# Optimization experiments

Hardware: AMD Instinct MI355X
Metric: run time of the kernel (lower is better)

## Reference

```python
import jax, jax.numpy as jnp
import numpy as np

DIM = 768
NUM_HEADS = 12
HEAD_DIM = DIM // NUM_HEADS
SCALE = HEAD_DIM ** -0.5
EPS = 1e-6


def setup_inputs() -> dict:
    key = jax.random.key(0)
    k_x, k_p, k_qkv, k_proj = jax.random.split(key, 4)
    B, N = 16, 577
    x = jax.random.normal(k_x, (B, N, DIM), dtype=jnp.float32)
    # binary keep/drop policy per token (as produced by an upstream gumbel gate)
    policy = jax.random.randint(k_p, (B, N, 1), 0, 2).astype(jnp.float32)
    Wqkv = jax.random.normal(k_qkv, (DIM, 3 * DIM), dtype=jnp.float32) * 0.02
    bqkv = jnp.zeros((3 * DIM,), dtype=jnp.float32)
    Wproj = jax.random.normal(k_proj, (DIM, DIM), dtype=jnp.float32) * 0.02
    bproj = jnp.zeros((DIM,), dtype=jnp.float32)
    return {"x": x, "policy": policy, "Wqkv": Wqkv, "bqkv": bqkv,
            "Wproj": Wproj, "bproj": bproj}


def reference(x, policy, Wqkv, bqkv, Wproj, bproj):
    B, N, C = x.shape
    # qkv projection -> [3, B, H, N, Dh]
    qkv = (x @ Wqkv + bqkv).reshape(B, N, 3, NUM_HEADS, HEAD_DIM)
    qkv = jnp.transpose(qkv, (2, 0, 3, 1, 4))
    q, k, v = qkv[0], qkv[1], qkv[2]
    # scaled attention logits [B, H, N, N]
    attn = jnp.einsum("bhnd,bhmd->bhnm", q, k) * SCALE
    # policy-masked softmax (training-mode formula: eye keeps self-attention alive)
    ap = policy.reshape(B, 1, 1, N)
    eye = jnp.eye(N, dtype=ap.dtype).reshape(1, 1, N, N)
    ap = ap + (1.0 - ap) * eye
    max_att = jnp.max(attn, axis=-1, keepdims=True)
    e = jnp.exp(attn - max_att) * ap
    attn = (e + EPS / N) / (jnp.sum(e, axis=-1, keepdims=True) + EPS)
    # attend and project
    out = jnp.einsum("bhnm,bhmd->bhnd", attn, v)
    out = jnp.transpose(out, (0, 2, 1, 3)).reshape(B, N, C)
    return out @ Wproj + bproj
```

## Files before the change

kernel.cpp:

```cpp
#include <hip/hip_runtime.h>
#include <hip/hip_bf16.h>

#define QKVC   2304
#define NHEAD  12
#define NTOK   577
#define NBATCH 16
#define NROWS  (NBATCH * NTOK)
#define NPAD   640
#define SCALE  0.125f
#define EPSV   1e-6f

typedef __bf16  bf16x8 __attribute__((ext_vector_type(8)));
typedef float   f32x4  __attribute__((ext_vector_type(4)));

__device__ __forceinline__ unsigned short f2bf(float f) {
    union { float f; unsigned u; } v; v.f = f;
    unsigned r = v.u + 0x7FFFu + ((v.u >> 16) & 1u);
    return (unsigned short)(r >> 16);
}
__device__ __forceinline__ unsigned short f2bf_trunc(float f) {
    return (unsigned short)(__float_as_uint(f) >> 16);
}
__device__ __forceinline__ f32x4 mfma16(bf16x8 a, bf16x8 b, f32x4 c) {
    return __builtin_amdgcn_mfma_f32_16x16x32_bf16(a, b, c, 0, 0, 0);
}

#define GLDS16(g, l) __builtin_amdgcn_global_load_lds( \
    (const __attribute__((address_space(1))) unsigned int*)(g), \
    (__attribute__((address_space(3))) unsigned int*)(l), 16, 0, 0)

__device__ void transpose_tile(const float* __restrict__ src, unsigned short* __restrict__ dst,
                               int K, int N, int bx, int by, int t) {
    __shared__ unsigned short lt[64 * 72];
    int n0 = bx * 64, k0 = by * 64;
    int kk = t >> 4, nn = (t & 15) * 4;
    for (int i = 0; i < 4; i++) {
        int kr = kk + i * 16;
        float4 v = *(const float4*)&src[(size_t)(k0 + kr) * N + n0 + nn];
        lt[(nn + 0) * 72 + kr] = f2bf(v.x);
        lt[(nn + 1) * 72 + kr] = f2bf(v.y);
        lt[(nn + 2) * 72 + kr] = f2bf(v.z);
        lt[(nn + 3) * 72 + kr] = f2bf(v.w);
    }
    __syncthreads();
    int n = t >> 2, seg = (t & 3) * 16;
    uint4 a = *(uint4*)&lt[n * 72 + seg];
    uint4 b = *(uint4*)&lt[n * 72 + seg + 8];
    *(uint4*)&dst[(size_t)(n0 + n) * K + k0 + seg]     = a;
    *(uint4*)&dst[(size_t)(n0 + n) * K + k0 + seg + 8] = b;
}

#define NCONV (NROWS * 768 / 4 / 256)
__global__ void k_prep(const float* __restrict__ x, unsigned short* __restrict__ xb,
                       const float* __restrict__ Wqkv, unsigned short* __restrict__ wqkvt,
                       const float* __restrict__ Wproj, unsigned short* __restrict__ wprojt) {
    int id = blockIdx.x, t = threadIdx.x;
    if (id < NCONV) {
        int idx = id * 256 + t;
        float4 v = ((const float4*)x)[idx];
        ushort4 o;
        o.x = f2bf(v.x); o.y = f2bf(v.y); o.z = f2bf(v.z); o.w = f2bf(v.w);
        ((ushort4*)xb)[idx] = o;
    } else if (id < NCONV + 432) {
        int i2 = id - NCONV;
        transpose_tile(Wqkv, wqkvt, 768, QKVC, i2 % 36, i2 / 36, t);
    } else {
        int i2 = id - NCONV - 432;
        transpose_tile(Wproj, wprojt, 768, 768, i2 % 12, i2 / 12, t);
    }
}

template <bool F32OUT>
__global__ __launch_bounds__(256, 3)
void k_gemm(const unsigned short* __restrict__ A, const unsigned short* __restrict__ B,
            const float* __restrict__ bias, void* __restrict__ outp, int Ncols,
            unsigned short* __restrict__ vt) {
    __shared__ unsigned short SL[24576];
    unsigned short (*As)[4096] = (unsigned short (*)[4096])SL;
    unsigned short (*Bs)[4096] = (unsigned short (*)[4096])&SL[12288];
    int t = threadIdx.x;
    int lane = t & 63, wave = t >> 6, quad = lane >> 4, l15 = lane & 15;
    int wm = wave >> 1, wn = wave & 1;
    int nT = Ncols >> 7;
    int mLocal = blockIdx.x & 7;
    int rest = blockIdx.x >> 3;
    int n0 = (rest % nT) * 128;
    int m0 = ((rest / nT) * 8 + mLocal) * 128;

    const unsigned short* ga0 = A + (size_t)(m0 + wave * 32 + (lane >> 2)) * 768 + (lane & 3) * 8;
    const unsigned short* ga1 = ga0 + (size_t)16 * 768;
    const unsigned short* gb0 = B + (size_t)(n0 + wave * 32 + (lane >> 2)) * 768 + (lane & 3) * 8;
    const unsigned short* gb1 = gb0 + (size_t)16 * 768;
    unsigned lo = wave * 1024;

    f32x4 acc[4][4] = {};

    GLDS16(ga0,      &As[0][lo]); GLDS16(ga1,      &As[0][lo + 512]);
    GLDS16(gb0,      &Bs[0][lo]); GLDS16(gb1,      &Bs[0][lo + 512]);
    GLDS16(ga0 + 32, &As[1][lo]); GLDS16(ga1 + 32, &As[1][lo + 512]);
    GLDS16(gb0 + 32, &Bs[1][lo]); GLDS16(gb1 + 32, &Bs[1][lo + 512]);

    #pragma unroll 3
    for (int kt = 0; kt < 24; kt++) {
        int buf = kt % 3;
        if (kt == 23) { asm volatile("s_waitcnt vmcnt(0)" ::: "memory"); }
        else          { asm volatile("s_waitcnt vmcnt(4)" ::: "memory"); }
        asm volatile("s_barrier" ::: "memory");
        if (kt < 22) {
            int nb = buf + 2; if (nb >= 3) nb -= 3;
            int ko = (kt + 2) * 32;
            GLDS16(ga0 + ko, &As[nb][lo]); GLDS16(ga1 + ko, &As[nb][lo + 512]);
            GLDS16(gb0 + ko, &Bs[nb][lo]); GLDS16(gb1 + ko, &Bs[nb][lo + 512]);
        }
        bf16x8 af[4], bfr[4];
        for (int i = 0; i < 4; i++) {
            af[i]  = *(const bf16x8*)&As[buf][(wm * 64 + i * 16 + l15) * 32 + quad * 8];
            bfr[i] = *(const bf16x8*)&Bs[buf][(wn * 64 + i * 16 + l15) * 32 + quad * 8];
        }
        for (int mi = 0; mi < 4; mi++)
            for (int ni = 0; ni < 4; ni++)
                acc[mi][ni] = mfma16(af[mi], bfr[ni], acc[mi][ni]);
    }
    asm volatile("" ::: "memory");

    if constexpr (F32OUT) {
        for (int ni = 0; ni < 4; ni++) {
            int col = n0 + wn * 64 + ni * 16 + l15;
            float bv = bias[col];
            for (int mi = 0; mi < 4; mi++) {
                int rowm = m0 + wm * 64 + mi * 16 + quad * 4;
                for (int r = 0; r < 4; r++) {
                    int m = rowm + r;
                    if (m < NROWS)
                        ((float*)outp)[(size_t)m * Ncols + col] = acc[mi][ni][r] + bv;
                }
            }
        }
    } else {
        __syncthreads();
        for (int ni = 0; ni < 4; ni++) {
            int colL = wn * 64 + ni * 16 + l15;
            float bv = bias[n0 + colL];
            for (int mi = 0; mi < 4; mi++) {
                int rowL = wm * 64 + mi * 16 + quad * 4;
                for (int r = 0; r < 4; r++)
                    SL[(rowL + r) * 132 + colL] = f2bf(acc[mi][ni][r] + bv);
            }
        }
        __syncthreads();
        if (n0 < 1536) {
            for (int rr = 0; rr < 8; rr++) {
                int row = rr * 16 + (t >> 4);
                int m = m0 + row;
                if (m < NROWS) {
                    uint4 v = *(uint4*)&SL[row * 132 + (t & 15) * 8];
                    *(uint4*)&((unsigned short*)outp)[(size_t)m * Ncols + n0 + (t & 15) * 8] = v;
                }
            }
        } else {
            int h0 = (n0 - 1536) >> 6;
            for (int i = 0; i < 32; i++) {
                int c = wave * 32 + i;
                int h = h0 + (c >> 6), d = c & 63;
                for (int half = 0; half < 2; half++) {
                    int lr = half * 64 + lane;
                    int m = m0 + lr;
                    if (m < NROWS) {
                        unsigned bb = (unsigned)m / 577u;
                        int tok = m - (int)bb * 577;
                        vt[(((size_t)bb * NHEAD + h) * 64 + d) * NPAD + tok] =
                            SL[lr * 132 + c];
                    }
                }
            }
        }
    }
}

__global__ __launch_bounds__(256, 4)
void k_attn(const unsigned short* __restrict__ qkv, const unsigned short* __restrict__ vt,
            const float* __restrict__ policy, unsigned short* __restrict__ ao) {
    __shared__ unsigned short Ks[64 * 72];
    __shared__ unsigned short Vs[64 * 72];
    __shared__ unsigned short Ps[4][32 * 72];
    __shared__ float pol[NPAD];
    int t = threadIdx.x;
    int lane = t & 63, wave = t >> 6, quad = lane >> 4, l15 = lane & 15;
    int b = blockIdx.z, h = blockIdx.y, qt = blockIdx.x;
    const unsigned short* qbase = qkv + (size_t)(b * NTOK) * QKVC + h * 64;
    const unsigned short* kbase = qkv + (size_t)(b * NTOK) * QKVC + 768 + h * 64;
    const unsigned short* vbase = vt + (size_t)(b * NHEAD + h) * 64 * NPAD;

    for (int i = t; i < NPAD; i += 256)
        pol[i] = (i < NTOK) ? policy[b * NTOK + i] : 0.f;

    bf16x8 qf[2][2];
    for (int mi = 0; mi < 2; mi++) {
        const unsigned short* qp =
            qbase + (size_t)(qt * 128 + mi * 64 + wave * 16 + l15) * QKVC + quad * 8;
        qf[mi][0] = *(const bf16x8*)qp;
        qf[mi][1] = *(const bf16x8*)(qp + 32);
    }
    bf16x8 onesf;
    for (int j = 0; j < 8; j++) onesf[j] = (__bf16)1.0f;
    f32x4 o[2][4] = {};
    f32x4 ls[2] = {};
    int rowtok0[2];
    for (int mi = 0; mi < 2; mi++)
        rowtok0[mi] = qt * 128 + mi * 64 + wave * 16 + quad * 4;
    __syncthreads();

    for (int kt = 0; kt < 10; kt++) {
        int key0 = kt * 64;
        for (int i = t; i < 512; i += 256) {
            int row = i >> 3, seg = (i & 7) * 8;
            *(uint4*)&Ks[row * 72 + seg] = *(const uint4*)&kbase[(size_t)(key0 + row) * QKVC + seg];
            *(uint4*)&Vs[row * 72 + seg] = *(const uint4*)&vbase[(size_t)row * NPAD + key0 + seg];
        }
        __syncthreads();

        for (int ci = 0; ci < 4; ci++) {
            bf16x8 kf0 = *(const bf16x8*)&Ks[(ci * 16 + l15) * 72 + quad * 8];
            bf16x8 kf1 = *(const bf16x8*)&Ks[(ci * 16 + l15) * 72 + 32 + quad * 8];
            int col = key0 + ci * 16 + l15;
            float pc = pol[col];
            for (int mi = 0; mi < 2; mi++) {
                f32x4 a = {};
                a = mfma16(qf[mi][0], kf0, a);
                a = mfma16(qf[mi][1], kf1, a);
                for (int r = 0; r < 4; r++) {
                    float ap = (col == rowtok0[mi] + r) ? 1.f : pc;
                    float e = __expf(a[r] * SCALE) * ap;
                    Ps[wave][(mi * 16 + quad * 4 + r) * 72 + ci * 16 + l15] = f2bf_trunc(e);
                }
            }
        }
        __asm__ volatile("s_waitcnt lgkmcnt(0)" ::: "memory");
        bf16x8 pf[2][2];
        for (int mi = 0; mi < 2; mi++) {
            pf[mi][0] = *(const bf16x8*)&Ps[wave][(mi * 16 + l15) * 72 + quad * 8];
            pf[mi][1] = *(const bf16x8*)&Ps[wave][(mi * 16 + l15) * 72 + 32 + quad * 8];
            ls[mi] = mfma16(pf[mi][0], onesf, ls[mi]);
            ls[mi] = mfma16(pf[mi][1], onesf, ls[mi]);
        }
        for (int di = 0; di < 4; di++) {
            bf16x8 vf0 = *(const bf16x8*)&Vs[(di * 16 + l15) * 72 + quad * 8];
            bf16x8 vf1 = *(const bf16x8*)&Vs[(di * 16 + l15) * 72 + 32 + quad * 8];
            for (int mi = 0; mi < 2; mi++) {
                o[mi][di] = mfma16(pf[mi][0], vf0, o[mi][di]);
                o[mi][di] = mfma16(pf[mi][1], vf1, o[mi][di]);
            }
        }
        __syncthreads();
    }

    for (int mi = 0; mi < 2; mi++) {
        for (int r = 0; r < 4; r++) {
            int tok = rowtok0[mi] + r;
            if (tok < NTOK) {
                float inv = __builtin_amdgcn_rcpf(ls[mi][r] + EPSV);
                for (int di = 0; di < 4; di++) {
                    float val = o[mi][di][r] * inv;
                    ao[((size_t)(b * NTOK + tok)) * 768 + h * 64 + di * 16 + l15] = f2bf(val);
                }
            }
        }
    }
}

extern "C" void kernel_launch(void* const* d_in, const int* in_sizes, int n_in,
                              void* d_out, int out_size, void* d_ws, size_t ws_size,
                              hipStream_t stream) {
    const float* x      = (const float*)d_in[0];
    const float* policy = (const float*)d_in[1];
    const float* Wqkv   = (const float*)d_in[2];
    const float* bqkv   = (const float*)d_in[3];
    const float* Wproj  = (const float*)d_in[4];
    const float* bproj  = (const float*)d_in[5];
    float* out = (float*)d_out;

    unsigned short* p = (unsigned short*)d_ws;
    unsigned short* xb     = p;
    unsigned short* ao     = p; p += (size_t)NROWS * 768;
    unsigned short* wqkvt  = p; p += (size_t)QKVC * 768;
    unsigned short* wprojt = p; p += (size_t)768 * 768;
    unsigned short* qkvb   = p; p += (size_t)NROWS * QKVC;
    unsigned short* vt     = p; p += (size_t)NBATCH * NHEAD * 64 * NPAD;

    int mT = (NROWS + 127) / 128;
    int mG = (mT + 7) / 8;

    k_prep<<<NCONV + 432 + 144, 256, 0, stream>>>(x, xb, Wqkv, wqkvt, Wproj, wprojt);
    k_gemm<false><<<mG * 8 * (QKVC / 128), 256, 0, stream>>>(
        xb, wqkvt, bqkv, (void*)qkvb, QKVC, vt);
    k_attn<<<dim3(NPAD / 128, NHEAD, NBATCH), 256, 0, stream>>>(qkvb, vt, policy, ao);
    k_gemm<true><<<mG * 8 * (768 / 128), 256, 0, stream>>>(
        ao, wprojt, bproj, (void*)out, 768, nullptr);
}
```

Measured before the change: 205.1 us.

## Switch GEMM to double-buffered K=64 stages with full vmcnt wait

The GEMM main loop moves from a triple-buffered K=32 pipeline with a partial vmcnt wait to a double-buffered K=64 pipeline that does half as many barrier iterations. Shared memory grows to 64 KB and the launch bound drops to 2 blocks per CU. The aim is to cut barrier and wait overhead per unit of MFMA work. The cost is lower occupancy and a full vmcnt(0) wait each iteration, so the next tile's load can no longer be in flight across the barrier.

```diff
diff --git a/kernel.cpp b/kernel.cpp
--- a/kernel.cpp
+++ b/kernel.cpp
@@ -71,13 +71,11 @@
 }
 
 template <bool F32OUT>
-__global__ __launch_bounds__(256, 3)
+__global__ __launch_bounds__(256, 2)
 void k_gemm(const unsigned short* __restrict__ A, const unsigned short* __restrict__ B,
             const float* __restrict__ bias, void* __restrict__ outp, int Ncols,
             unsigned short* __restrict__ vt) {
-    __shared__ unsigned short SL[24576];
-    unsigned short (*As)[4096] = (unsigned short (*)[4096])SL;
-    unsigned short (*Bs)[4096] = (unsigned short (*)[4096])&SL[12288];
+    __shared__ unsigned short SL[32768];
     int t = threadIdx.x;
     int lane = t & 63, wave = t >> 6, quad = lane >> 4, l15 = lane & 15;
     int wm = wave >> 1, wn = wave & 1;
@@ -95,31 +93,35 @@
 
     f32x4 acc[4][4] = {};
 
-    GLDS16(ga0,      &As[0][lo]); GLDS16(ga1,      &As[0][lo + 512]);
-    GLDS16(gb0,      &Bs[0][lo]); GLDS16(gb1,      &Bs[0][lo + 512]);
-    GLDS16(ga0 + 32, &As[1][lo]); GLDS16(ga1 + 32, &As[1][lo + 512]);
-    GLDS16(gb0 + 32, &Bs[1][lo]); GLDS16(gb1 + 32, &Bs[1][lo + 512]);
-
-    #pragma unroll 3
-    for (int kt = 0; kt < 24; kt++) {
-        int buf = kt % 3;
-        if (kt == 23) { asm volatile("s_waitcnt vmcnt(0)" ::: "memory"); }
-        else          { asm volatile("s_waitcnt vmcnt(4)" ::: "memory"); }
+    GLDS16(ga0,      &SL[lo]);              GLDS16(ga1,      &SL[lo + 512]);
+    GLDS16(ga0 + 32, &SL[4096 + lo]);       GLDS16(ga1 + 32, &SL[4096 + lo + 512]);
+    GLDS16(gb0,      &SL[16384 + lo]);      GLDS16(gb1,      &SL[16384 + lo + 512]);
+    GLDS16(gb0 + 32, &SL[20480 + lo]);      GLDS16(gb1 + 32, &SL[20480 + lo + 512]);
+
+    #pragma unroll 2
+    for (int kt = 0; kt < 12; kt++) {
+        unsigned ab = (kt & 1) * 8192;
+        unsigned bb = 16384 + ab;
+        asm volatile("s_waitcnt vmcnt(0)" ::: "memory");
         asm volatile("s_barrier" ::: "memory");
-        if (kt < 22) {
-            int nb = buf + 2; if (nb >= 3) nb -= 3;
-            int ko = (kt + 2) * 32;
-            GLDS16(ga0 + ko, &As[nb][lo]); GLDS16(ga1 + ko, &As[nb][lo + 512]);
-            GLDS16(gb0 + ko, &Bs[nb][lo]); GLDS16(gb1 + ko, &Bs[nb][lo + 512]);
-        }
-        bf16x8 af[4], bfr[4];
-        for (int i = 0; i < 4; i++) {
-            af[i]  = *(const bf16x8*)&As[buf][(wm * 64 + i * 16 + l15) * 32 + quad * 8];
-            bfr[i] = *(const bf16x8*)&Bs[buf][(wn * 64 + i * 16 + l15) * 32 + quad * 8];
-        }
-        for (int mi = 0; mi < 4; mi++)
-            for (int ni = 0; ni < 4; ni++)
-                acc[mi][ni] = mfma16(af[mi], bfr[ni], acc[mi][ni]);
+        if (kt < 11) {
+            unsigned na = 8192 - ab, nb = 16384 + na;
+            int ko = (kt + 1) * 64;
+            GLDS16(ga0 + ko,      &SL[na + lo]);        GLDS16(ga1 + ko,      &SL[na + lo + 512]);
+            GLDS16(ga0 + ko + 32, &SL[na + 4096 + lo]); GLDS16(ga1 + ko + 32, &SL[na + 4096 + lo + 512]);
+            GLDS16(gb0 + ko,      &SL[nb + lo]);        GLDS16(gb1 + ko,      &SL[nb + lo + 512]);
+            GLDS16(gb0 + ko + 32, &SL[nb + 4096 + lo]); GLDS16(gb1 + ko + 32, &SL[nb + 4096 + lo + 512]);
+        }
+        for (int h = 0; h < 2; h++) {
+            bf16x8 af[4], bfr[4];
+            for (int i = 0; i < 4; i++) {
+                af[i]  = *(const bf16x8*)&SL[ab + h * 4096 + (wm * 64 + i * 16 + l15) * 32 + quad * 8];
+                bfr[i] = *(const bf16x8*)&SL[bb + h * 4096 + (wn * 64 + i * 16 + l15) * 32 + quad * 8];
+            }
+            for (int mi = 0; mi < 4; mi++)
+                for (int ni = 0; ni < 4; ni++)
+                    acc[mi][ni] = mfma16(af[mi], bfr[ni], acc[mi][ni]);
+        }
     }
     asm volatile("" ::: "memory");
 
@@ -166,9 +168,9 @@
                     int lr = half * 64 + lane;
                     int m = m0 + lr;
                     if (m < NROWS) {
-                        unsigned bb = (unsigned)m / 577u;
-                        int tok = m - (int)bb * 577;
-                        vt[(((size_t)bb * NHEAD + h) * 64 + d) * NPAD + tok] =
+                        unsigned bbx = (unsigned)m / 577u;
+                        int tok = m - (int)bbx * 577;
+                        vt[(((size_t)bbx * NHEAD + h) * 64 + d) * NPAD + tok] =
                             SL[lr * 132 + c];
                     }
                 }
```

Result: no change. 204.0 us (-0.5%).
